# Performance work log

Measured on AMD Instinct MI355X. Metric: run time of the kernel, lower is better.

## Reference

```python
import jax, jax.numpy as jnp
import numpy as np

H = 768
B = 65536
T = 3
EPS = 1e-5


def setup_inputs() -> dict:
    key = jax.random.key(0)
    ks = jax.random.split(key, 6)
    s = 1.0 / np.sqrt(H)
    return {
        "features": jax.random.normal(ks[0], (B, T, H), dtype=jnp.float32),
        "Wq": jax.random.normal(ks[1], (H, H), dtype=jnp.float32) * s,
        "bq": jnp.zeros((H,), jnp.float32),
        "Wk": jax.random.normal(ks[2], (H, H), dtype=jnp.float32) * s,
        "bk": jnp.zeros((H,), jnp.float32),
        "Wv": jax.random.normal(ks[3], (H, H), dtype=jnp.float32) * s,
        "bv": jnp.zeros((H,), jnp.float32),
        "Wo": jax.random.normal(ks[4], (H, H), dtype=jnp.float32) * s,
        "bo": jnp.zeros((H,), jnp.float32),
        "ln_g": jnp.ones((H,), jnp.float32),
        "ln_b": jnp.zeros((H,), jnp.float32),
    }


def reference(features, Wq, bq, Wk, bk, Wv, bv, Wo, bo, ln_g, ln_b):
    # LayerNorm over last dim
    mu = jnp.mean(features, axis=-1, keepdims=True)
    var = jnp.mean(jnp.square(features - mu), axis=-1, keepdims=True)
    x = (features - mu) * jax.lax.rsqrt(var + EPS) * ln_g + ln_b  # [B,T,H]

    scale = H ** (-0.5)
    Q = jnp.einsum("bth,oh->bto", x, Wq) + bq
    K = jnp.einsum("bth,oh->bto", x, Wk) + bk
    V = jnp.einsum("bth,oh->bto", x, Wv) + bv

    Qp, Qn = jax.nn.relu(Q), jax.nn.relu(-Q)
    Kp, Kn = jax.nn.relu(K), jax.nn.relu(-K)

    attn_pos = jax.nn.softmax(jnp.einsum("bqh,bkh->bqk", Qp, Kp) * scale, axis=-1)
    attn_neg = jax.nn.softmax(jnp.einsum("bqh,bkh->bqk", Qn, Kn) * scale, axis=-1)

    out = jnp.einsum("bqk,bkh->bqh", attn_pos, V) - jnp.einsum("bqk,bkh->bqh", attn_neg, V)
    out = jnp.einsum("bth,oh->bto", out, Wo) + bo
    return x + out
```

## Files before the change

kernel.cpp:

```cpp
#include <hip/hip_runtime.h>

typedef __attribute__((ext_vector_type(8))) _Float16 half8;
typedef __attribute__((ext_vector_type(4))) _Float16 half4;
typedef __attribute__((ext_vector_type(4))) float f32x4;

#define HDIM 768
#define LNEPS 1e-5f

#define L_AS   0
#define L_BS   24576
#define L_STQ  57344
#define L_STK  108032
#define L_SP   158720
#define L_SN   161024
#define L_TOT  163328
#define SSTR   264

__device__ __forceinline__ void gload_lds16(const void* g, void* l) {
  __builtin_amdgcn_global_load_lds(
      (const __attribute__((address_space(1))) void*)g,
      (__attribute__((address_space(3))) void*)l, 16, 0, 0);
}

__global__ __launch_bounds__(256) void convert_kernel(
    const float* __restrict__ Wq, const float* __restrict__ Wk,
    const float* __restrict__ bq, const float* __restrict__ bk,
    _Float16* __restrict__ Wf, float* __restrict__ biasf)
{
  const long NW = 1536L * 768;
  long i = (long)blockIdx.x * 256 + threadIdx.x;
  if (i < NW) {
    const int orow = (int)(i / 768);
    const int k = (int)(i - (long)orow * 768);
    const int n = orow >> 8, c = orow & 255;
    const int src = n * 128 + (c & 127);
    Wf[i] = (_Float16)((c < 128) ? Wq[(long)src * 768 + k]
                                 : Wk[(long)src * 768 + k]);
  } else if (i < NW + 1536) {
    const int j = (int)(i - NW);
    const int n = j >> 8, c = j & 255;
    const int src = n * 128 + (c & 127);
    biasf[j] = (c < 128) ? bq[src] : bk[src];
  }
}

__global__ __launch_bounds__(256) void wvo_kernel(
    const float* __restrict__ Wo, const float* __restrict__ Wv,
    const float* __restrict__ bv,
    _Float16* __restrict__ Wvo, float* __restrict__ bvo)
{
  if (blockIdx.x == 144) {
    for (int o = threadIdx.x; o < 768; o += 256) {
      float s = 0.f;
      for (int h = 0; h < 768; ++h) s += Wo[o * 768 + h] * bv[h];
      bvo[o] = s;
    }
    return;
  }
  __shared__ float As[64][65];
  __shared__ float Bs[64][65];
  const int bm = blockIdx.x / 12, bn = blockIdx.x % 12;
  const int tid = threadIdx.x;
  const int tr = tid >> 4, tc = tid & 15;
  float acc[4][4] = {};
  for (int k0 = 0; k0 < 768; k0 += 64) {
    __syncthreads();
#pragma unroll
    for (int i = 0; i < 16; ++i) {
      const int e = i * 256 + tid, r = e >> 6, c = e & 63;
      As[r][c] = Wo[(bm * 64 + r) * 768 + (k0 + c)];
      Bs[r][c] = Wv[(k0 + r) * 768 + (bn * 64 + c)];
    }
    __syncthreads();
#pragma unroll 8
    for (int k = 0; k < 64; ++k) {
      float a[4], b[4];
#pragma unroll
      for (int i = 0; i < 4; ++i) a[i] = As[tr * 4 + i][k];
#pragma unroll
      for (int j = 0; j < 4; ++j) b[j] = Bs[k][tc * 4 + j];
#pragma unroll
      for (int i = 0; i < 4; ++i)
#pragma unroll
        for (int j = 0; j < 4; ++j) acc[i][j] += a[i] * b[j];
    }
  }
#pragma unroll
  for (int i = 0; i < 4; ++i)
#pragma unroll
    for (int j = 0; j < 4; ++j)
      Wvo[(bm * 64 + tr * 4 + i) * 768 + bn * 64 + tc * 4 + j] = (_Float16)acc[i][j];
}

__global__ __launch_bounds__(256) void ln_kernel(
    const float* __restrict__ feat, const float* __restrict__ gamma,
    const float* __restrict__ beta, _Float16* __restrict__ xout)
{
  const int w = threadIdx.x >> 6, lane = threadIdx.x & 63;
  const long row = (long)blockIdx.x * 4 + w;
  const float* fr = feat + row * HDIM;
  float4 v[3];
  float s = 0.f, ss = 0.f;
#pragma unroll
  for (int i = 0; i < 3; ++i) {
    v[i] = *(const float4*)&fr[(i * 64 + lane) * 4];
    s  += v[i].x + v[i].y + v[i].z + v[i].w;
    ss += v[i].x * v[i].x + v[i].y * v[i].y + v[i].z * v[i].z + v[i].w * v[i].w;
  }
#pragma unroll
  for (int off = 32; off; off >>= 1) {
    s  += __shfl_xor(s, off);
    ss += __shfl_xor(ss, off);
  }
  const float mu = s * (1.f / 768.f);
  const float var = ss * (1.f / 768.f) - mu * mu;
  const float rs = rsqrtf(var + LNEPS);
#pragma unroll
  for (int i = 0; i < 3; ++i) {
    const int idx = (i * 64 + lane) * 4;
    float4 g4 = *(const float4*)&gamma[idx];
    float4 b4 = *(const float4*)&beta[idx];
    half4 o;
    o[0] = (_Float16)((v[i].x - mu) * rs * g4.x + b4.x);
    o[1] = (_Float16)((v[i].y - mu) * rs * g4.y + b4.y);
    o[2] = (_Float16)((v[i].z - mu) * rs * g4.z + b4.z);
    o[3] = (_Float16)((v[i].w - mu) * rs * g4.w + b4.w);
    *(half4*)&xout[row * HDIM + idx] = o;
  }
}

__global__ __launch_bounds__(512, 1) void fused_kernel(
    const _Float16* __restrict__ xh,
    const _Float16* __restrict__ Wf,
    const float* __restrict__ bias,
    const float* __restrict__ bo,
    float* __restrict__ out)
{
  __shared__ __align__(16) char lds[L_TOT];
  const int tid = threadIdx.x;
  const int lane = tid & 63;
  const int quad = lane >> 4, l16 = lane & 15;
  const int w = tid >> 6;
  const int wm = w >> 2, wn = w & 3;

  const int nwg = gridDim.x;
  const int orig = blockIdx.x;
  const int bid = (orig & 7) * (nwg >> 3) + (orig >> 3);
  const long m0 = (long)bid * 192;

  {
    float* sc = (float*)(lds + L_SP);
#pragma unroll
    for (int i = 0; i < 3; ++i) {
      const int idx = i * 512 + tid;
      if (idx < 1152) sc[idx] = 0.f;
    }
  }

  const int wg = w & 3;
  long aOff[3]; int aLds[3];
#pragma unroll
  for (int i = 0; i < 3; ++i) {
    const int c = i * 256 + wg * 64 + lane, r = c >> 2, p = c & 3;
    const int cc = p ^ ((r >> 1) & 3);
    aOff[i] = (m0 + r) * HDIM + cc * 8;
    aLds[i] = c * 16;
  }
  long bOff[4]; int bLds[4];
#pragma unroll
  for (int i = 0; i < 4; ++i) {
    const int c = i * 256 + wg * 64 + lane, r = c >> 2, p = c & 3;
    const int cc = p ^ ((r >> 1) & 3);
    bOff[i] = (long)r * HDIM + cc * 8;
    bLds[i] = c * 16;
  }

  int stg_buf = 0; long stg_k = 0; long stg_nb = 0;
#define STAGE()                                                               \
  do {                                                                        \
    if (w < 4) {                                                              \
      _Pragma("unroll")                                                       \
      for (int i_ = 0; i_ < 3; ++i_)                                          \
        gload_lds16(xh + aOff[i_] + stg_k, lds + L_AS + stg_buf * 12288 + aLds[i_]); \
    } else {                                                                  \
      _Pragma("unroll")                                                       \
      for (int i_ = 0; i_ < 4; ++i_)                                          \
        gload_lds16(Wf + stg_nb + bOff[i_] + stg_k, lds + L_BS + stg_buf * 16384 + bLds[i_]); \
    }                                                                         \
    stg_buf ^= 1; stg_k += 32;                                                \
    if (stg_k == HDIM) { stg_k = 0; stg_nb += 256L * HDIM; }                  \
  } while (0)
#define VMW()                                                                 \
  do { if (w < 4) { asm volatile("s_waitcnt vmcnt(3)" ::: "memory"); }        \
       else       { asm volatile("s_waitcnt vmcnt(4)" ::: "memory"); } } while (0)

  f32x4 acc[6][4];
#pragma unroll
  for (int mi = 0; mi < 6; ++mi)
#pragma unroll
    for (int ni = 0; ni < 4; ++ni)
#pragma unroll
      for (int j = 0; j < 4; ++j) acc[mi][ni][j] = 0.f;

  STAGE(); STAGE();
  VMW();
  __builtin_amdgcn_s_barrier();
  __builtin_amdgcn_sched_barrier(0);

  for (int n = 0; n < 9; ++n) {
    for (int ks = 0; ks < 24; ++ks) {
      const int s = n * 24 + ks;
      const int buf = s & 1;
      const char* as = lds + L_AS + buf * 12288;
      const char* bs = lds + L_BS + buf * 16384;
      half8 af[6], bf[4];
#pragma unroll
      for (int mi = 0; mi < 6; ++mi) {
        const int r = wm * 96 + mi * 16 + l16;
        af[mi] = *(const half8*)(as + r * 64 + ((quad ^ ((r >> 1) & 3)) * 16));
      }
#pragma unroll
      for (int ni = 0; ni < 4; ++ni) {
        const int r = wn * 64 + ni * 16 + l16;
        bf[ni] = *(const half8*)(bs + r * 64 + ((quad ^ ((r >> 1) & 3)) * 16));
      }
      __builtin_amdgcn_s_setprio(1);
#pragma unroll
      for (int mi = 0; mi < 6; ++mi)
#pragma unroll
        for (int ni = 0; ni < 4; ++ni)
          acc[mi][ni] = __builtin_amdgcn_mfma_f32_16x16x32_f16(af[mi], bf[ni], acc[mi][ni], 0, 0, 0);
      __builtin_amdgcn_s_setprio(0);
      __builtin_amdgcn_sched_barrier(0);
      __builtin_amdgcn_s_barrier();
      __builtin_amdgcn_sched_barrier(0);
      if (s + 2 < 216) STAGE();
      if (s < 214) {
        VMW();
        __builtin_amdgcn_s_barrier();
        __builtin_amdgcn_sched_barrier(0);
      } else if (s == 214) {
        asm volatile("s_waitcnt vmcnt(0)" ::: "memory");
        __builtin_amdgcn_s_barrier();
        __builtin_amdgcn_sched_barrier(0);
      }
    }

    {
      float bv[4];
#pragma unroll
      for (int ni = 0; ni < 4; ++ni)
        bv[ni] = bias[n * 256 + wn * 64 + ni * 16 + l16];
      char* st = lds + ((wn >> 1) ? L_STK : L_STQ);
      const int cb = (wn & 1) * 64;
#pragma unroll
      for (int mi = 0; mi < 6; ++mi)
#pragma unroll
        for (int ni = 0; ni < 4; ++ni)
#pragma unroll
          for (int j = 0; j < 4; ++j) {
            const int row = wm * 96 + mi * 16 + quad * 4 + j;
            *(_Float16*)(st + row * SSTR + (cb + ni * 16 + l16) * 2) =
                (_Float16)(acc[mi][ni][j] + bv[ni]);
          }
#pragma unroll
      for (int mi = 0; mi < 6; ++mi)
#pragma unroll
        for (int ni = 0; ni < 4; ++ni)
#pragma unroll
          for (int j = 0; j < 4; ++j) acc[mi][ni][j] = 0.f;
    }
    __builtin_amdgcn_s_barrier();

    if (n < 6) {
      const int b = tid >> 3, sub = tid & 7;
      half4 qv[3][4], kv[3][4];
#pragma unroll
      for (int t = 0; t < 3; ++t) {
        const char* rq = lds + L_STQ + (3 * b + t) * SSTR + sub * 32;
        const char* rk = lds + L_STK + (3 * b + t) * SSTR + sub * 32;
#pragma unroll
        for (int u = 0; u < 4; ++u) {
          qv[t][u] = *(const half4*)(rq + u * 8);
          kv[t][u] = *(const half4*)(rk + u * 8);
        }
      }
#pragma unroll
      for (int qi = 0; qi < 3; ++qi)
#pragma unroll
        for (int ki = 0; ki < 3; ++ki) {
          float p = 0.f, nn = 0.f;
#pragma unroll
          for (int u = 0; u < 4; ++u)
#pragma unroll
            for (int e = 0; e < 4; ++e) {
              const float qq = (float)qv[qi][u][e];
              const float kk = (float)kv[ki][u][e];
              p  += fmaxf(qq, 0.f) * fmaxf(kk, 0.f);
              nn += fminf(qq, 0.f) * fminf(kk, 0.f);
            }
          p  += __shfl_xor(p, 1);  p  += __shfl_xor(p, 2);  p  += __shfl_xor(p, 4);
          nn += __shfl_xor(nn, 1); nn += __shfl_xor(nn, 2); nn += __shfl_xor(nn, 4);
          if (sub == 0) {
            ((float*)(lds + L_SP))[b * 9 + qi * 3 + ki] += p;
            ((float*)(lds + L_SN))[b * 9 + qi * 3 + ki] += nn;
          }
        }
      __builtin_amdgcn_s_barrier();
      if (n == 5) {
        if (tid < 64) {
          float* sp = (float*)(lds + L_SP) + tid * 9;
          float* sn = (float*)(lds + L_SN) + tid * 9;
          const float scale = 0.03608439182435161f;
#pragma unroll
          for (int qi = 0; qi < 3; ++qi) {
            const float p0 = sp[qi*3+0]*scale, p1 = sp[qi*3+1]*scale, p2 = sp[qi*3+2]*scale;
            const float n0 = sn[qi*3+0]*scale, n1 = sn[qi*3+1]*scale, n2 = sn[qi*3+2]*scale;
            const float mp = fmaxf(p0, fmaxf(p1, p2));
            const float mn = fmaxf(n0, fmaxf(n1, n2));
            const float ep0 = __expf(p0-mp), ep1 = __expf(p1-mp), ep2 = __expf(p2-mp);
            const float en0 = __expf(n0-mn), en1 = __expf(n1-mn), en2 = __expf(n2-mn);
            const float rp = 1.f / (ep0+ep1+ep2), rn = 1.f / (en0+en1+en2);
            sp[qi*3+0] = ep0*rp - en0*rn;
            sp[qi*3+1] = ep1*rp - en1*rn;
            sp[qi*3+2] = ep2*rp - en2*rn;
          }
        }
        __builtin_amdgcn_s_barrier();
      }
    } else {
      const int cg = tid & 63, rg = tid >> 6;
      const int c = cg * 4;
      const char* vb = lds + ((c >> 7) ? L_STK : L_STQ) + (c & 127) * 2;
      const long gc = 256L * (n - 6) + c;
      const f32x4 bov = *(const f32x4*)&bo[gc];
      const float* cf0 = (const float*)(lds + L_SP);
#pragma unroll 4
      for (int rr = 0; rr < 24; ++rr) {
        const int row = rr * 8 + rg;
        const int b = (int)((unsigned)row / 3u);
        const int t = row - 3 * b;
        const float* cf = cf0 + b * 9 + t * 3;
        const half4 v0 = *(const half4*)(vb + (3 * b + 0) * SSTR);
        const half4 v1 = *(const half4*)(vb + (3 * b + 1) * SSTR);
        const half4 v2 = *(const half4*)(vb + (3 * b + 2) * SSTR);
        const half4 hx = *(const half4*)&xh[(m0 + row) * HDIM + gc];
        const float c0 = cf[0], c1 = cf[1], c2 = cf[2];
        f32x4 o;
#pragma unroll
        for (int j = 0; j < 4; ++j)
          o[j] = (float)hx[j] + bov[j] + c0 * (float)v0[j]
               + c1 * (float)v1[j] + c2 * (float)v2[j];
        *(f32x4*)&out[(m0 + row) * HDIM + gc] = o;
      }
      __builtin_amdgcn_s_barrier();
    }
  }
#undef STAGE
#undef VMW
}

extern "C" void kernel_launch(void* const* d_in, const int* in_sizes, int n_in,
                              void* d_out, int out_size, void* d_ws, size_t ws_size,
                              hipStream_t stream) {
  (void)in_sizes; (void)n_in; (void)out_size; (void)ws_size;
  const float* feat = (const float*)d_in[0];
  const float* Wq   = (const float*)d_in[1];
  const float* bq   = (const float*)d_in[2];
  const float* Wk   = (const float*)d_in[3];
  const float* bk   = (const float*)d_in[4];
  const float* Wv   = (const float*)d_in[5];
  const float* bv   = (const float*)d_in[6];
  const float* Wo   = (const float*)d_in[7];
  const float* bo   = (const float*)d_in[8];
  const float* ln_g = (const float*)d_in[9];
  const float* ln_b = (const float*)d_in[10];

  char* ws = (char*)d_ws;
  _Float16* xh    = (_Float16*)(ws);
  _Float16* Wf    = (_Float16*)(ws + 301989888L);
  float*    biasf = (float*)   (ws + 305528832L);

  convert_kernel<<<4614, 256, 0, stream>>>(Wq, Wk, bq, bk, Wf, biasf);
  wvo_kernel<<<145, 256, 0, stream>>>(Wo, Wv, bv, Wf + 1536L * 768, biasf + 1536);
  ln_kernel<<<49152, 256, 0, stream>>>(feat, ln_g, ln_b, xh);
  fused_kernel<<<1024, 512, 0, stream>>>(xh, Wf, biasf, bo, (float*)d_out);
}
```

Measured before the change: 1.285 ms.

## Compute attention scores and output epilogue directly from MFMA registers, shrinking LDS

Q and K weight rows are interleaved so each lane's Q/K pair sits in neighbouring lanes. Score dot products are then reduced with shuffles straight from the accumulators, and the V/output epilogue combines accumulators with the softmax coefficients in registers. A rows are permuted at load time so each wave holds whole token triples. This removes the fp16 staging buffers in LDS and several barriers, cutting LDS use enough to drop the one-block-per-CU launch bound. It also drops the V bias term, which cancels because the pos and neg attention rows each sum to one. The cost is more shuffle and register pressure and narrower, per-element global stores for the output.

```diff
diff --git a/kernel.cpp b/kernel.cpp
--- a/kernel.cpp
+++ b/kernel.cpp
@@ -7,14 +7,11 @@
 #define HDIM 768
 #define LNEPS 1e-5f
 
-#define L_AS   0
-#define L_BS   24576
-#define L_STQ  57344
-#define L_STK  108032
-#define L_SP   158720
-#define L_SN   161024
-#define L_TOT  163328
-#define SSTR   264
+#define L_A    0
+#define L_B    24576
+#define L_SP   57344
+#define L_SN   66560
+#define L_TOT  75776
 
 __device__ __forceinline__ void gload_lds16(const void* g, void* l) {
   __builtin_amdgcn_global_load_lds(
@@ -32,31 +29,19 @@
   if (i < NW) {
     const int orow = (int)(i / 768);
     const int k = (int)(i - (long)orow * 768);
-    const int n = orow >> 8, c = orow & 255;
-    const int src = n * 128 + (c & 127);
-    Wf[i] = (_Float16)((c < 128) ? Wq[(long)src * 768 + k]
-                                 : Wk[(long)src * 768 + k]);
+    const int h = orow >> 1;
+    Wf[i] = (_Float16)((orow & 1) ? Wk[(long)h * 768 + k] : Wq[(long)h * 768 + k]);
   } else if (i < NW + 1536) {
     const int j = (int)(i - NW);
-    const int n = j >> 8, c = j & 255;
-    const int src = n * 128 + (c & 127);
-    biasf[j] = (c < 128) ? bq[src] : bk[src];
+    const int h = j >> 1;
+    biasf[j] = (j & 1) ? bk[h] : bq[h];
   }
 }
 
 __global__ __launch_bounds__(256) void wvo_kernel(
     const float* __restrict__ Wo, const float* __restrict__ Wv,
-    const float* __restrict__ bv,
-    _Float16* __restrict__ Wvo, float* __restrict__ bvo)
+    _Float16* __restrict__ Wvo)
 {
-  if (blockIdx.x == 144) {
-    for (int o = threadIdx.x; o < 768; o += 256) {
-      float s = 0.f;
-      for (int h = 0; h < 768; ++h) s += Wo[o * 768 + h] * bv[h];
-      bvo[o] = s;
-    }
-    return;
-  }
   __shared__ float As[64][65];
   __shared__ float Bs[64][65];
   const int bm = blockIdx.x / 12, bn = blockIdx.x % 12;
@@ -129,10 +114,10 @@
   }
 }
 
-__global__ __launch_bounds__(512, 1) void fused_kernel(
+__global__ __launch_bounds__(512) void fused_kernel(
     const _Float16* __restrict__ xh,
     const _Float16* __restrict__ Wf,
-    const float* __restrict__ bias,
+    const float* __restrict__ biasf,
     const float* __restrict__ bo,
     float* __restrict__ out)
 {
@@ -151,9 +136,9 @@
   {
     float* sc = (float*)(lds + L_SP);
 #pragma unroll
-    for (int i = 0; i < 3; ++i) {
+    for (int i = 0; i < 9; ++i) {
       const int idx = i * 512 + tid;
-      if (idx < 1152) sc[idx] = 0.f;
+      if (idx < 4608) sc[idx] = 0.f;
     }
   }
 
@@ -163,7 +148,10 @@
   for (int i = 0; i < 3; ++i) {
     const int c = i * 256 + wg * 64 + lane, r = c >> 2, p = c & 3;
     const int cc = p ^ ((r >> 1) & 3);
-    aOff[i] = (m0 + r) * HDIM + cc * 8;
+    const int top = r / 96, r2 = r % 96;
+    const int grp = r2 / 48, t = (r2 % 48) / 16, bl = r2 % 16;
+    const long grow = m0 + 3L * (top * 32 + grp * 16 + bl) + t;
+    aOff[i] = grow * HDIM + cc * 8;
     aLds[i] = c * 16;
   }
   long bOff[4]; int bLds[4];
@@ -181,11 +169,11 @@
     if (w < 4) {                                                              \
       _Pragma("unroll")                                                       \
       for (int i_ = 0; i_ < 3; ++i_)                                          \
-        gload_lds16(xh + aOff[i_] + stg_k, lds + L_AS + stg_buf * 12288 + aLds[i_]); \
+        gload_lds16(xh + aOff[i_] + stg_k, lds + L_A + stg_buf * 12288 + aLds[i_]); \
     } else {                                                                  \
       _Pragma("unroll")                                                       \
       for (int i_ = 0; i_ < 4; ++i_)                                          \
-        gload_lds16(Wf + stg_nb + bOff[i_] + stg_k, lds + L_BS + stg_buf * 16384 + bLds[i_]); \
+        gload_lds16(Wf + stg_nb + bOff[i_] + stg_k, lds + L_B + stg_buf * 16384 + bLds[i_]); \
     }                                                                         \
     stg_buf ^= 1; stg_k += 32;                                                \
     if (stg_k == HDIM) { stg_k = 0; stg_nb += 256L * HDIM; }                  \
@@ -193,6 +181,7 @@
 #define VMW()                                                                 \
   do { if (w < 4) { asm volatile("s_waitcnt vmcnt(3)" ::: "memory"); }        \
        else       { asm volatile("s_waitcnt vmcnt(4)" ::: "memory"); } } while (0)
+#define SB0() __builtin_amdgcn_sched_barrier(0)
 
   f32x4 acc[6][4];
 #pragma unroll
@@ -205,14 +194,14 @@
   STAGE(); STAGE();
   VMW();
   __builtin_amdgcn_s_barrier();
-  __builtin_amdgcn_sched_barrier(0);
-
-  for (int n = 0; n < 9; ++n) {
+  SB0();
+
+  for (int nt = 0; nt < 9; ++nt) {
     for (int ks = 0; ks < 24; ++ks) {
-      const int s = n * 24 + ks;
+      const int s = nt * 24 + ks;
       const int buf = s & 1;
-      const char* as = lds + L_AS + buf * 12288;
-      const char* bs = lds + L_BS + buf * 16384;
+      const char* as = lds + L_A + buf * 12288;
+      const char* bs = lds + L_B + buf * 16384;
       half8 af[6], bf[4];
 #pragma unroll
       for (int mi = 0; mi < 6; ++mi) {
@@ -231,133 +220,160 @@
         for (int ni = 0; ni < 4; ++ni)
           acc[mi][ni] = __builtin_amdgcn_mfma_f32_16x16x32_f16(af[mi], bf[ni], acc[mi][ni], 0, 0, 0);
       __builtin_amdgcn_s_setprio(0);
-      __builtin_amdgcn_sched_barrier(0);
+      SB0();
       __builtin_amdgcn_s_barrier();
-      __builtin_amdgcn_sched_barrier(0);
+      SB0();
       if (s + 2 < 216) STAGE();
       if (s < 214) {
         VMW();
         __builtin_amdgcn_s_barrier();
-        __builtin_amdgcn_sched_barrier(0);
+        SB0();
       } else if (s == 214) {
         asm volatile("s_waitcnt vmcnt(0)" ::: "memory");
         __builtin_amdgcn_s_barrier();
-        __builtin_amdgcn_sched_barrier(0);
+        SB0();
       }
     }
 
-    {
-      float bv[4];
+    if (nt < 6) {
+      float bc[4];
 #pragma unroll
       for (int ni = 0; ni < 4; ++ni)
-        bv[ni] = bias[n * 256 + wn * 64 + ni * 16 + l16];
-      char* st = lds + ((wn >> 1) ? L_STK : L_STQ);
-      const int cb = (wn & 1) * 64;
-#pragma unroll
-      for (int mi = 0; mi < 6; ++mi)
+        bc[ni] = biasf[nt * 256 + wn * 64 + ni * 16 + l16];
+#pragma unroll
+      for (int g = 0; g < 2; ++g) {
+        float pp[3][3][4], nn[3][3][4];
+#pragma unroll
+        for (int qi = 0; qi < 3; ++qi)
+#pragma unroll
+          for (int ki = 0; ki < 3; ++ki)
+#pragma unroll
+            for (int j = 0; j < 4; ++j) { pp[qi][ki][j] = 0.f; nn[qi][ki][j] = 0.f; }
 #pragma unroll
         for (int ni = 0; ni < 4; ++ni)
 #pragma unroll
           for (int j = 0; j < 4; ++j) {
-            const int row = wm * 96 + mi * 16 + quad * 4 + j;
-            *(_Float16*)(st + row * SSTR + (cb + ni * 16 + l16) * 2) =
-                (_Float16)(acc[mi][ni][j] + bv[ni]);
+            float v[3], vp[3];
+#pragma unroll
+            for (int t = 0; t < 3; ++t) {
+              v[t] = acc[g * 3 + t][ni][j] + bc[ni];
+              vp[t] = __shfl_xor(v[t], 1);
+            }
+#pragma unroll
+            for (int qi = 0; qi < 3; ++qi)
+#pragma unroll
+              for (int ki = 0; ki < 3; ++ki) {
+                pp[qi][ki][j] += fmaxf(v[qi], 0.f) * fmaxf(vp[ki], 0.f);
+                nn[qi][ki][j] += fminf(v[qi], 0.f) * fminf(vp[ki], 0.f);
+              }
           }
 #pragma unroll
-      for (int mi = 0; mi < 6; ++mi)
-#pragma unroll
-        for (int ni = 0; ni < 4; ++ni)
-#pragma unroll
-          for (int j = 0; j < 4; ++j) acc[mi][ni][j] = 0.f;
-    }
-    __builtin_amdgcn_s_barrier();
-
-    if (n < 6) {
-      const int b = tid >> 3, sub = tid & 7;
-      half4 qv[3][4], kv[3][4];
-#pragma unroll
-      for (int t = 0; t < 3; ++t) {
-        const char* rq = lds + L_STQ + (3 * b + t) * SSTR + sub * 32;
-        const char* rk = lds + L_STK + (3 * b + t) * SSTR + sub * 32;
-#pragma unroll
-        for (int u = 0; u < 4; ++u) {
-          qv[t][u] = *(const half4*)(rq + u * 8);
-          kv[t][u] = *(const half4*)(rk + u * 8);
-        }
-      }
-#pragma unroll
-      for (int qi = 0; qi < 3; ++qi)
-#pragma unroll
-        for (int ki = 0; ki < 3; ++ki) {
-          float p = 0.f, nn = 0.f;
-#pragma unroll
-          for (int u = 0; u < 4; ++u)
-#pragma unroll
-            for (int e = 0; e < 4; ++e) {
-              const float qq = (float)qv[qi][u][e];
-              const float kk = (float)kv[ki][u][e];
-              p  += fmaxf(qq, 0.f) * fmaxf(kk, 0.f);
-              nn += fminf(qq, 0.f) * fminf(kk, 0.f);
+        for (int qi = 0; qi < 3; ++qi)
+#pragma unroll
+          for (int ki = 0; ki < 3; ++ki)
+#pragma unroll
+            for (int j = 0; j < 4; ++j) {
+              float p = pp[qi][ki][j], nnn = nn[qi][ki][j];
+              p += __shfl_xor(p, 2); nnn += __shfl_xor(nnn, 2);
+              p += __shfl_xor(p, 4); nnn += __shfl_xor(nnn, 4);
+              p += __shfl_xor(p, 8); nnn += __shfl_xor(nnn, 8);
+              pp[qi][ki][j] = p; nn[qi][ki][j] = nnn;
             }
-          p  += __shfl_xor(p, 1);  p  += __shfl_xor(p, 2);  p  += __shfl_xor(p, 4);
-          nn += __shfl_xor(nn, 1); nn += __shfl_xor(nn, 2); nn += __shfl_xor(nn, 4);
-          if (sub == 0) {
-            ((float*)(lds + L_SP))[b * 9 + qi * 3 + ki] += p;
-            ((float*)(lds + L_SN))[b * 9 + qi * 3 + ki] += nn;
+        if (l16 == 0) {
+          float* sps = (float*)(lds + L_SP) + wn * 576;
+          float* sns = (float*)(lds + L_SN) + wn * 576;
+#pragma unroll
+          for (int j = 0; j < 4; ++j) {
+            const int b = wm * 32 + g * 16 + quad * 4 + j;
+#pragma unroll
+            for (int qi = 0; qi < 3; ++qi)
+#pragma unroll
+              for (int ki = 0; ki < 3; ++ki) {
+                sps[b * 9 + qi * 3 + ki] += pp[qi][ki][j];
+                sns[b * 9 + qi * 3 + ki] += nn[qi][ki][j];
+              }
           }
         }
-      __builtin_amdgcn_s_barrier();
-      if (n == 5) {
+      }
+#pragma unroll
+      for (int mi = 0; mi < 6; ++mi)
+#pragma unroll
+        for (int ni = 0; ni < 4; ++ni)
+#pragma unroll
+          for (int j = 0; j < 4; ++j) acc[mi][ni][j] = 0.f;
+
+      if (nt == 5) {
+        __builtin_amdgcn_s_barrier();
         if (tid < 64) {
-          float* sp = (float*)(lds + L_SP) + tid * 9;
-          float* sn = (float*)(lds + L_SN) + tid * 9;
+          const int b = tid;
+          float sp9[9], sn9[9];
+#pragma unroll
+          for (int k = 0; k < 9; ++k) { sp9[k] = 0.f; sn9[k] = 0.f; }
+#pragma unroll
+          for (int sl = 0; sl < 4; ++sl)
+#pragma unroll
+            for (int k = 0; k < 9; ++k) {
+              sp9[k] += ((float*)(lds + L_SP))[sl * 576 + b * 9 + k];
+              sn9[k] += ((float*)(lds + L_SN))[sl * 576 + b * 9 + k];
+            }
           const float scale = 0.03608439182435161f;
+          float* cf = (float*)(lds + L_SP) + b * 9;
 #pragma unroll
           for (int qi = 0; qi < 3; ++qi) {
-            const float p0 = sp[qi*3+0]*scale, p1 = sp[qi*3+1]*scale, p2 = sp[qi*3+2]*scale;
-            const float n0 = sn[qi*3+0]*scale, n1 = sn[qi*3+1]*scale, n2 = sn[qi*3+2]*scale;
+            const float p0 = sp9[qi*3+0]*scale, p1 = sp9[qi*3+1]*scale, p2 = sp9[qi*3+2]*scale;
+            const float n0 = sn9[qi*3+0]*scale, n1 = sn9[qi*3+1]*scale, n2 = sn9[qi*3+2]*scale;
             const float mp = fmaxf(p0, fmaxf(p1, p2));
             const float mn = fmaxf(n0, fmaxf(n1, n2));
             const float ep0 = __expf(p0-mp), ep1 = __expf(p1-mp), ep2 = __expf(p2-mp);
             const float en0 = __expf(n0-mn), en1 = __expf(n1-mn), en2 = __expf(n2-mn);
             const float rp = 1.f / (ep0+ep1+ep2), rn = 1.f / (en0+en1+en2);
-            sp[qi*3+0] = ep0*rp - en0*rn;
-            sp[qi*3+1] = ep1*rp - en1*rn;
-            sp[qi*3+2] = ep2*rp - en2*rn;
+            cf[qi*3+0] = ep0*rp - en0*rn;
+            cf[qi*3+1] = ep1*rp - en1*rn;
+            cf[qi*3+2] = ep2*rp - en2*rn;
           }
         }
         __builtin_amdgcn_s_barrier();
       }
     } else {
-      const int cg = tid & 63, rg = tid >> 6;
-      const int c = cg * 4;
-      const char* vb = lds + ((c >> 7) ? L_STK : L_STQ) + (c & 127) * 2;
-      const long gc = 256L * (n - 6) + c;
-      const f32x4 bov = *(const f32x4*)&bo[gc];
+      int gc[4]; float boc[4];
+#pragma unroll
+      for (int ni = 0; ni < 4; ++ni) {
+        gc[ni] = (nt - 6) * 256 + wn * 64 + ni * 16 + l16;
+        boc[ni] = bo[gc[ni]];
+      }
       const float* cf0 = (const float*)(lds + L_SP);
-#pragma unroll 4
-      for (int rr = 0; rr < 24; ++rr) {
-        const int row = rr * 8 + rg;
-        const int b = (int)((unsigned)row / 3u);
-        const int t = row - 3 * b;
-        const float* cf = cf0 + b * 9 + t * 3;
-        const half4 v0 = *(const half4*)(vb + (3 * b + 0) * SSTR);
-        const half4 v1 = *(const half4*)(vb + (3 * b + 1) * SSTR);
-        const half4 v2 = *(const half4*)(vb + (3 * b + 2) * SSTR);
-        const half4 hx = *(const half4*)&xh[(m0 + row) * HDIM + gc];
-        const float c0 = cf[0], c1 = cf[1], c2 = cf[2];
-        f32x4 o;
-#pragma unroll
-        for (int j = 0; j < 4; ++j)
-          o[j] = (float)hx[j] + bov[j] + c0 * (float)v0[j]
-               + c1 * (float)v1[j] + c2 * (float)v2[j];
-        *(f32x4*)&out[(m0 + row) * HDIM + gc] = o;
-      }
-      __builtin_amdgcn_s_barrier();
+#pragma unroll
+      for (int g = 0; g < 2; ++g)
+#pragma unroll
+        for (int j = 0; j < 4; ++j) {
+          const int b = wm * 32 + g * 16 + quad * 4 + j;
+          float c9[9];
+#pragma unroll
+          for (int k = 0; k < 9; ++k) c9[k] = cf0[b * 9 + k];
+#pragma unroll
+          for (int t = 0; t < 3; ++t) {
+            const long row = m0 + 3L * b + t;
+#pragma unroll
+            for (int ni = 0; ni < 4; ++ni) {
+              const float val = (float)xh[row * HDIM + gc[ni]] + boc[ni]
+                  + c9[t*3+0] * acc[g*3+0][ni][j]
+                  + c9[t*3+1] * acc[g*3+1][ni][j]
+                  + c9[t*3+2] * acc[g*3+2][ni][j];
+              out[row * HDIM + gc[ni]] = val;
+            }
+          }
+        }
+#pragma unroll
+      for (int mi = 0; mi < 6; ++mi)
+#pragma unroll
+        for (int ni = 0; ni < 4; ++ni)
+#pragma unroll
+          for (int j = 0; j < 4; ++j) acc[mi][ni][j] = 0.f;
     }
   }
 #undef STAGE
 #undef VMW
+#undef SB0
 }
 
 extern "C" void kernel_launch(void* const* d_in, const int* in_sizes, int n_in,
@@ -375,6 +391,7 @@
   const float* bo   = (const float*)d_in[8];
   const float* ln_g = (const float*)d_in[9];
   const float* ln_b = (const float*)d_in[10];
+  (void)bv;
 
   char* ws = (char*)d_ws;
   _Float16* xh    = (_Float16*)(ws);
@@ -382,7 +399,7 @@
   float*    biasf = (float*)   (ws + 305528832L);
 
   convert_kernel<<<4614, 256, 0, stream>>>(Wq, Wk, bq, bk, Wf, biasf);
-  wvo_kernel<<<145, 256, 0, stream>>>(Wo, Wv, bv, Wf + 1536L * 768, biasf + 1536);
+  wvo_kernel<<<144, 256, 0, stream>>>(Wo, Wv, Wf + 1536L * 768);
   ln_kernel<<<49152, 256, 0, stream>>>(feat, ln_g, ln_b, xh);
   fused_kernel<<<1024, 512, 0, stream>>>(xh, Wf, biasf, bo, (float*)d_out);
 }
```

Result: slower. 1.997 ms (+55.4%).
